# Optimization experiments

Measured on AMD Instinct MI355X. Metric: run time of the kernel, lower is better.

## Reference

```python
import jax, jax.numpy as jnp
import numpy as np

N_QUBITS = 8
EMBED_DIM = 1024
FFN_DIM = 4096


def _apply_1q_batched(state, gate, wire):
    # state: [N] + [2]*n ; gate: [N,2,2] (per-sample)
    n = state.ndim - 1
    N = state.shape[0]
    L = 2 ** wire
    R = 2 ** (n - 1 - wire)
    st = state.reshape(N, L, 2, R)
    st = jnp.einsum('nba,nlar->nlbr', gate, st)
    return st.reshape((N,) + (2,) * n)


def _apply_1q_shared(state, gate, wire):
    # gate: [2,2] shared across samples
    n = state.ndim - 1
    N = state.shape[0]
    L = 2 ** wire
    R = 2 ** (n - 1 - wire)
    st = state.reshape(N, L, 2, R)
    st = jnp.einsum('ba,nlar->nlbr', gate, st)
    return st.reshape((N,) + (2,) * n)


def _cnot(state, control, target):
    c_ax = control + 1
    t_ax = target + 1
    s0 = jnp.take(state, 0, axis=c_ax)
    s1 = jnp.take(state, 1, axis=c_ax)
    t_ax2 = t_ax - 1 if t_ax > c_ax else t_ax  # axis shift after take
    s1 = jnp.flip(s1, axis=t_ax2)
    return jnp.stack([s0, s1], axis=c_ax)


def _simulate(q_inputs, qparams):
    # q_inputs: [N, n_qubits] RX angles; qparams: [n_qubits, 3] Rot(phi,theta,omega)
    N = q_inputs.shape[0]
    n = N_QUBITS
    state = jnp.zeros((N, 2 ** n), dtype=jnp.complex64).at[:, 0].set(1.0)
    state = state.reshape((N,) + (2,) * n)
    # RX layer (per-sample angles)
    half = q_inputs.astype(jnp.float32) * 0.5
    c = jnp.cos(half).astype(jnp.complex64)
    s = (-1j) * jnp.sin(half).astype(jnp.complex64)
    for i in range(n):
        gate = jnp.stack([jnp.stack([c[:, i], s[:, i]], -1),
                          jnp.stack([s[:, i], c[:, i]], -1)], -2)  # [N,2,2]
        state = _apply_1q_batched(state, gate, i)
    # Rot layer: Rot(phi, theta, omega) = RZ(omega) RY(theta) RZ(phi)
    for i in range(n):
        phi, theta, omega = qparams[i, 0], qparams[i, 1], qparams[i, 2]
        ct = jnp.cos(theta / 2).astype(jnp.complex64)
        st = jnp.sin(theta / 2).astype(jnp.complex64)
        ep = jnp.exp(-0.5j * (phi + omega).astype(jnp.complex64))
        em = jnp.exp(0.5j * (phi - omega).astype(jnp.complex64))
        gate = jnp.array(0., jnp.complex64) + jnp.stack([
            jnp.stack([ep * ct, -em * st]),
            jnp.stack([jnp.conj(em) * st, jnp.conj(ep) * ct])])
        state = _apply_1q_shared(state, gate, i)
    # CNOT ring
    for i in range(n - 1):
        state = _cnot(state, i, i + 1)
    state = _cnot(state, n - 1, 0)
    # PauliZ expectations
    probs = jnp.abs(state) ** 2  # [N] + [2]*n, float32
    zs = []
    for i in range(n):
        axes = tuple(a for a in range(1, n + 1) if a != i + 1)
        m = probs.sum(axes)  # [N,2]
        zs.append(m[:, 0] - m[:, 1])
    return jnp.stack(zs, -1)  # [N, n_qubits]


def setup_inputs() -> dict:
    key = jax.random.key(0)
    k = jax.random.split(key, 6)
    x = jax.random.normal(k[0], (4, 2048, EMBED_DIM), dtype=jnp.float32)
    W1 = jax.random.normal(k[1], (FFN_DIM, EMBED_DIM), dtype=jnp.float32) * 0.02
    b1 = jnp.zeros((FFN_DIM,), dtype=jnp.float32)
    qparams = jax.random.normal(k[2], (N_QUBITS, 3), dtype=jnp.float32)
    W2 = jax.random.normal(k[3], (EMBED_DIM, N_QUBITS), dtype=jnp.float32) * 0.02
    b2 = jnp.zeros((EMBED_DIM,), dtype=jnp.float32)
    return {"x": x, "W1": W1, "b1": b1, "qparams": qparams, "W2": W2, "b2": b2}


def reference(x, W1, b1, qparams, W2, b2):
    batch, seq_len, embed_dim = x.shape
    x_flat = x.reshape(-1, embed_dim)
    x_ffn = x_flat @ W1.T + b1                       # [N, ffn_dim]
    q_inputs = x_ffn[:, :N_QUBITS]                   # ffn_dim >= n_qubits
    q_out = _simulate(q_inputs, qparams)             # [N, n_qubits]
    out = q_out @ W2.T + b2                          # [N, embed_dim]
    return out.reshape(batch, seq_len, embed_dim)
```

## Files before the change

### kernel.cpp

```cpp
#include <hip/hip_runtime.h>
#include <math.h>


constexpr int EMBED = 1024;
constexpr int NQ    = 8;
constexpr int BLOCK = 256;
constexpr int WAVES = BLOCK / 64;
constexpr int RPW   = 4;
constexpr float INV2PI = 0.15915494309189535f;

__global__ __launch_bounds__(BLOCK, 2)
void ffq(const float* __restrict__ x,
         const float* __restrict__ W1,
         const float* __restrict__ b1,
         const float* __restrict__ qp,
         const float* __restrict__ W2,
         const float* __restrict__ b2,
         float* __restrict__ out,
         int total_rows)
{
    const int t    = threadIdx.x;
    const int lane = t & 63;
    const int wv   = t >> 6;

    __shared__ float lds_w1[NQ * EMBED];

    {
        const float4* src = reinterpret_cast<const float4*>(W1);
        float4* dst = reinterpret_cast<float4*>(lds_w1);
#pragma unroll
        for (int k = 0; k < (NQ * EMBED / 4) / BLOCK; ++k)
            dst[k * BLOCK + t] = src[k * BLOCK + t];
    }

    const int j = lane & 7;
    float Rj, qoffj;
    {
        const float phi = qp[j * 3 + 0];
        const float th  = qp[j * 3 + 1];
        const float cth  = cosf(th);
        const float ssps = sinf(th) * sinf(phi);
        Rj    = sqrtf(cth * cth + ssps * ssps);
        qoffj = (b1[j] + atan2f(ssps, cth)) * INV2PI;
    }

    float4 w2a[4][4], w2b[4][4];
    float4 b2f[4];
#pragma unroll
    for (int i = 0; i < 4; ++i) {
        const int c = i * 256 + lane * 4;
#pragma unroll
        for (int q = 0; q < 4; ++q) {
            w2a[i][q] = *reinterpret_cast<const float4*>(W2 + (c + q) * NQ);
            w2b[i][q] = *reinterpret_cast<const float4*>(W2 + (c + q) * NQ + 4);
        }
        b2f[i] = *reinterpret_cast<const float4*>(b2 + c);
    }

    __syncthreads();

    const int  gw = blockIdx.x * WAVES + wv;
    const long r0 = (long)gw * RPW;

    float4 xv[4];
    if (r0 < total_rows) {
#pragma unroll
        for (int i = 0; i < 4; ++i)
            xv[i] = *reinterpret_cast<const float4*>(
                x + (size_t)r0 * EMBED + i * 256 + lane * 4);
    }

    for (int rr = 0; rr < RPW; ++rr) {
        const long row = r0 + rr;
        if (row >= total_rows) break;

        float4 xn[4];
        const bool more = (rr + 1 < RPW) && (row + 1 < total_rows);
        if (more) {
#pragma unroll
            for (int i = 0; i < 4; ++i)
                xn[i] = *reinterpret_cast<const float4*>(
                    x + (size_t)(row + 1) * EMBED + i * 256 + lane * 4);
        }

        float p[NQ];
#pragma unroll
        for (int jj = 0; jj < NQ; ++jj) p[jj] = 0.f;
#pragma unroll
        for (int i = 0; i < 4; ++i) {
#pragma unroll
            for (int jj = 0; jj < NQ; ++jj) {
                const float4 w = *reinterpret_cast<const float4*>(
                    lds_w1 + jj * EMBED + i * 256 + lane * 4);
                p[jj] += xv[i].x * w.x + xv[i].y * w.y +
                         xv[i].z * w.z + xv[i].w * w.w;
            }
        }

        float q4[4], q2[2], tsum;
        {
            const bool up = (lane & 4);
#pragma unroll
            for (int k = 0; k < 4; ++k) {
                const float snd = up ? p[k]     : p[k + 4];
                const float kp  = up ? p[k + 4] : p[k];
                q4[k] = kp + __shfl_xor(snd, 4, 64);
            }
        }
        {
            const bool up = (lane & 2);
#pragma unroll
            for (int k = 0; k < 2; ++k) {
                const float snd = up ? q4[k]     : q4[k + 2];
                const float kp  = up ? q4[k + 2] : q4[k];
                q2[k] = kp + __shfl_xor(snd, 2, 64);
            }
        }
        {
            const bool up = (lane & 1);
            const float snd = up ? q2[0] : q2[1];
            const float kp  = up ? q2[1] : q2[0];
            tsum = kp + __shfl_xor(snd, 1, 64);
        }
        tsum += __shfl_xor(tsum, 8, 64);
        tsum += __shfl_xor(tsum, 16, 64);
        tsum += __shfl_xor(tsum, 32, 64);

        const float arg = tsum * INV2PI + qoffj;
        const float zz  = Rj * __builtin_amdgcn_cosf(arg);

        float z0_, z1_, z2_, z3_, z4_, z5_, z6_, z7_;
        {
            const float o  = __shfl_xor(zz, 1, 64);
            const float a0 = (lane & 1) ? o  : zz;
            const float a1 = (lane & 1) ? zz : o;
            const float rA = __shfl_xor(a0, 2, 64);
            const float rB = __shfl_xor(a1, 2, 64);
            const float c0 = (lane & 2) ? rA : a0;
            const float c1 = (lane & 2) ? rB : a1;
            const float c2 = (lane & 2) ? a0 : rA;
            const float c3 = (lane & 2) ? a1 : rB;
            const float d0 = __shfl_xor(c0, 4, 64);
            const float d1 = __shfl_xor(c1, 4, 64);
            const float d2 = __shfl_xor(c2, 4, 64);
            const float d3 = __shfl_xor(c3, 4, 64);
            z0_ = (lane & 4) ? d0 : c0;
            z1_ = (lane & 4) ? d1 : c1;
            z2_ = (lane & 4) ? d2 : c2;
            z3_ = (lane & 4) ? d3 : c3;
            z4_ = (lane & 4) ? c0 : d0;
            z5_ = (lane & 4) ? c1 : d1;
            z6_ = (lane & 4) ? c2 : d2;
            z7_ = (lane & 4) ? c3 : d3;
        }

        float qo0, qo1, qo2, qo3, qo4, qo5, qo6, qo7;
        qo1 = z0_ * z1_;
        qo2 = qo1 * z2_;
        qo3 = qo2 * z3_;
        qo4 = qo3 * z4_;
        qo5 = qo4 * z5_;
        qo6 = qo5 * z6_;
        qo7 = qo6 * z7_;
        qo0 = z1_ * z2_ * z3_ * z4_ * z5_ * z6_ * z7_;

        float* outp = out + (size_t)row * EMBED;
#pragma unroll
        for (int i = 0; i < 4; ++i) {
            float4 o = b2f[i];
            o.x += qo0 * w2a[i][0].x + qo1 * w2a[i][0].y + qo2 * w2a[i][0].z + qo3 * w2a[i][0].w
                 + qo4 * w2b[i][0].x + qo5 * w2b[i][0].y + qo6 * w2b[i][0].z + qo7 * w2b[i][0].w;
            o.y += qo0 * w2a[i][1].x + qo1 * w2a[i][1].y + qo2 * w2a[i][1].z + qo3 * w2a[i][1].w
                 + qo4 * w2b[i][1].x + qo5 * w2b[i][1].y + qo6 * w2b[i][1].z + qo7 * w2b[i][1].w;
            o.z += qo0 * w2a[i][2].x + qo1 * w2a[i][2].y + qo2 * w2a[i][2].z + qo3 * w2a[i][2].w
                 + qo4 * w2b[i][2].x + qo5 * w2b[i][2].y + qo6 * w2b[i][2].z + qo7 * w2b[i][2].w;
            o.w += qo0 * w2a[i][3].x + qo1 * w2a[i][3].y + qo2 * w2a[i][3].z + qo3 * w2a[i][3].w
                 + qo4 * w2b[i][3].x + qo5 * w2b[i][3].y + qo6 * w2b[i][3].z + qo7 * w2b[i][3].w;
            *reinterpret_cast<float4*>(outp + i * 256 + lane * 4) = o;
        }

#pragma unroll
        for (int i = 0; i < 4; ++i) xv[i] = xn[i];
    }
}

extern "C" void kernel_launch(void* const* d_in, const int* in_sizes, int n_in,
                              void* d_out, int out_size, void* d_ws, size_t ws_size,
                              hipStream_t stream) {
    const float* x  = (const float*)d_in[0];
    const float* W1 = (const float*)d_in[1];
    const float* b1 = (const float*)d_in[2];
    const float* qp = (const float*)d_in[3];
    const float* W2 = (const float*)d_in[4];
    const float* b2 = (const float*)d_in[5];
    float* out = (float*)d_out;

    const int rows = in_sizes[0] / EMBED;
    const int rows_per_block = WAVES * RPW;
    const int grid = (rows + rows_per_block - 1) / rows_per_block;

    hipLaunchKernelGGL(ffq, dim3(grid), dim3(BLOCK), 0, stream,
                       x, W1, b1, qp, W2, b2, out, rows);
}
```

Before: 108.1 us.

## Batch four rows per wave and stage transposed W2 in LDS

Each wave now issues all four rows' x loads up front, before the W1 staging, and processes the rows jointly. Every W1 LDS read feeds four rows of FMAs, and W2 is transposed into LDS instead of being held in 32 float4 registers per thread. This aims to get more memory parallelism early and to cut register pressure and LDS traffic per row. The cost is doubled LDS use per block (64KB), which may limit occupancy, plus more live x registers and extra transpose work at block start.

```diff
diff --git a/kernel.cpp b/kernel.cpp
--- a/kernel.cpp
+++ b/kernel.cpp
@@ -5,8 +5,8 @@
 constexpr int EMBED = 1024;
 constexpr int NQ    = 8;
 constexpr int BLOCK = 256;
-constexpr int WAVES = BLOCK / 64;
 constexpr int RPW   = 4;
+constexpr int BR    = 16;
 constexpr float INV2PI = 0.15915494309189535f;
 
 __global__ __launch_bounds__(BLOCK, 2)
@@ -22,88 +22,90 @@
     const int t    = threadIdx.x;
     const int lane = t & 63;
     const int wv   = t >> 6;
-
-    __shared__ float lds_w1[NQ * EMBED];
+    const int j    = lane & 7;
+
+    __shared__ float w1s[NQ * EMBED];
+    __shared__ float w2t[NQ * EMBED];
+
+    const long r0 = (long)blockIdx.x * BR + wv * RPW;
+
+    float4 xv[RPW][4];
+#pragma unroll
+    for (int r = 0; r < RPW; ++r) {
+        long row = r0 + r; if (row >= total_rows) row = total_rows - 1;
+#pragma unroll
+        for (int i = 0; i < 4; ++i)
+            xv[r][i] = *reinterpret_cast<const float4*>(
+                x + (size_t)row * EMBED + i * 256 + lane * 4);
+    }
 
     {
-        const float4* src = reinterpret_cast<const float4*>(W1);
-        float4* dst = reinterpret_cast<float4*>(lds_w1);
+        const float4* w1g = reinterpret_cast<const float4*>(W1);
+        float4* w1d = reinterpret_cast<float4*>(w1s);
 #pragma unroll
         for (int k = 0; k < (NQ * EMBED / 4) / BLOCK; ++k)
-            dst[k * BLOCK + t] = src[k * BLOCK + t];
-    }
-
-    const int j = lane & 7;
+            w1d[k * BLOCK + t] = w1g[k * BLOCK + t];
+#pragma unroll
+        for (int m = 0; m < 4; ++m) {
+            const int col = m * BLOCK + t;
+            const float4 a = *reinterpret_cast<const float4*>(W2 + col * NQ);
+            const float4 b = *reinterpret_cast<const float4*>(W2 + col * NQ + 4);
+            w2t[0 * EMBED + col] = a.x;  w2t[1 * EMBED + col] = a.y;
+            w2t[2 * EMBED + col] = a.z;  w2t[3 * EMBED + col] = a.w;
+            w2t[4 * EMBED + col] = b.x;  w2t[5 * EMBED + col] = b.y;
+            w2t[6 * EMBED + col] = b.z;  w2t[7 * EMBED + col] = b.w;
+        }
+    }
+
     float Rj, qoffj;
     {
-        const float phi = qp[j * 3 + 0];
-        const float th  = qp[j * 3 + 1];
+        const float phi  = qp[j * 3 + 0];
+        const float th   = qp[j * 3 + 1];
         const float cth  = cosf(th);
         const float ssps = sinf(th) * sinf(phi);
         Rj    = sqrtf(cth * cth + ssps * ssps);
         qoffj = (b1[j] + atan2f(ssps, cth)) * INV2PI;
     }
 
-    float4 w2a[4][4], w2b[4][4];
-    float4 b2f[4];
+    float4 b2v[4];
+#pragma unroll
+    for (int i = 0; i < 4; ++i)
+        b2v[i] = *reinterpret_cast<const float4*>(b2 + i * 256 + lane * 4);
+
+    __syncthreads();
+
+    float p[RPW][NQ];
+#pragma unroll
+    for (int r = 0; r < RPW; ++r)
+#pragma unroll
+        for (int jj = 0; jj < NQ; ++jj) p[r][jj] = 0.f;
+
 #pragma unroll
     for (int i = 0; i < 4; ++i) {
-        const int c = i * 256 + lane * 4;
-#pragma unroll
-        for (int q = 0; q < 4; ++q) {
-            w2a[i][q] = *reinterpret_cast<const float4*>(W2 + (c + q) * NQ);
-            w2b[i][q] = *reinterpret_cast<const float4*>(W2 + (c + q) * NQ + 4);
-        }
-        b2f[i] = *reinterpret_cast<const float4*>(b2 + c);
-    }
-
-    __syncthreads();
-
-    const int  gw = blockIdx.x * WAVES + wv;
-    const long r0 = (long)gw * RPW;
-
-    float4 xv[4];
-    if (r0 < total_rows) {
-#pragma unroll
-        for (int i = 0; i < 4; ++i)
-            xv[i] = *reinterpret_cast<const float4*>(
-                x + (size_t)r0 * EMBED + i * 256 + lane * 4);
-    }
-
-    for (int rr = 0; rr < RPW; ++rr) {
-        const long row = r0 + rr;
-        if (row >= total_rows) break;
-
-        float4 xn[4];
-        const bool more = (rr + 1 < RPW) && (row + 1 < total_rows);
-        if (more) {
-#pragma unroll
-            for (int i = 0; i < 4; ++i)
-                xn[i] = *reinterpret_cast<const float4*>(
-                    x + (size_t)(row + 1) * EMBED + i * 256 + lane * 4);
-        }
-
-        float p[NQ];
-#pragma unroll
-        for (int jj = 0; jj < NQ; ++jj) p[jj] = 0.f;
-#pragma unroll
-        for (int i = 0; i < 4; ++i) {
-#pragma unroll
-            for (int jj = 0; jj < NQ; ++jj) {
-                const float4 w = *reinterpret_cast<const float4*>(
-                    lds_w1 + jj * EMBED + i * 256 + lane * 4);
-                p[jj] += xv[i].x * w.x + xv[i].y * w.y +
-                         xv[i].z * w.z + xv[i].w * w.w;
-            }
-        }
-
+#pragma unroll
+        for (int jj = 0; jj < NQ; ++jj) {
+            const float4 w = *reinterpret_cast<const float4*>(
+                w1s + jj * EMBED + i * 256 + lane * 4);
+#pragma unroll
+            for (int r = 0; r < RPW; ++r) {
+                p[r][jj] = fmaf(xv[r][i].x, w.x, p[r][jj]);
+                p[r][jj] = fmaf(xv[r][i].y, w.y, p[r][jj]);
+                p[r][jj] = fmaf(xv[r][i].z, w.z, p[r][jj]);
+                p[r][jj] = fmaf(xv[r][i].w, w.w, p[r][jj]);
+            }
+        }
+    }
+
+    float qo[RPW][NQ];
+#pragma unroll
+    for (int r = 0; r < RPW; ++r) {
         float q4[4], q2[2], tsum;
         {
             const bool up = (lane & 4);
 #pragma unroll
             for (int k = 0; k < 4; ++k) {
-                const float snd = up ? p[k]     : p[k + 4];
-                const float kp  = up ? p[k + 4] : p[k];
+                const float snd = up ? p[r][k]     : p[r][k + 4];
+                const float kp  = up ? p[r][k + 4] : p[r][k];
                 q4[k] = kp + __shfl_xor(snd, 4, 64);
             }
         }
@@ -126,8 +128,7 @@
         tsum += __shfl_xor(tsum, 16, 64);
         tsum += __shfl_xor(tsum, 32, 64);
 
-        const float arg = tsum * INV2PI + qoffj;
-        const float zz  = Rj * __builtin_amdgcn_cosf(arg);
+        const float zz = Rj * __builtin_amdgcn_cosf(tsum * INV2PI + qoffj);
 
         float z0_, z1_, z2_, z3_, z4_, z5_, z6_, z7_;
         {
@@ -154,33 +155,39 @@
             z7_ = (lane & 4) ? c3 : d3;
         }
 
-        float qo0, qo1, qo2, qo3, qo4, qo5, qo6, qo7;
-        qo1 = z0_ * z1_;
-        qo2 = qo1 * z2_;
-        qo3 = qo2 * z3_;
-        qo4 = qo3 * z4_;
-        qo5 = qo4 * z5_;
-        qo6 = qo5 * z6_;
-        qo7 = qo6 * z7_;
-        qo0 = z1_ * z2_ * z3_ * z4_ * z5_ * z6_ * z7_;
-
-        float* outp = out + (size_t)row * EMBED;
-#pragma unroll
-        for (int i = 0; i < 4; ++i) {
-            float4 o = b2f[i];
-            o.x += qo0 * w2a[i][0].x + qo1 * w2a[i][0].y + qo2 * w2a[i][0].z + qo3 * w2a[i][0].w
-                 + qo4 * w2b[i][0].x + qo5 * w2b[i][0].y + qo6 * w2b[i][0].z + qo7 * w2b[i][0].w;
-            o.y += qo0 * w2a[i][1].x + qo1 * w2a[i][1].y + qo2 * w2a[i][1].z + qo3 * w2a[i][1].w
-                 + qo4 * w2b[i][1].x + qo5 * w2b[i][1].y + qo6 * w2b[i][1].z + qo7 * w2b[i][1].w;
-            o.z += qo0 * w2a[i][2].x + qo1 * w2a[i][2].y + qo2 * w2a[i][2].z + qo3 * w2a[i][2].w
-                 + qo4 * w2b[i][2].x + qo5 * w2b[i][2].y + qo6 * w2b[i][2].z + qo7 * w2b[i][2].w;
-            o.w += qo0 * w2a[i][3].x + qo1 * w2a[i][3].y + qo2 * w2a[i][3].z + qo3 * w2a[i][3].w
-                 + qo4 * w2b[i][3].x + qo5 * w2b[i][3].y + qo6 * w2b[i][3].z + qo7 * w2b[i][3].w;
-            *reinterpret_cast<float4*>(outp + i * 256 + lane * 4) = o;
-        }
-
-#pragma unroll
-        for (int i = 0; i < 4; ++i) xv[i] = xn[i];
+        qo[r][1] = z0_ * z1_;
+        qo[r][2] = qo[r][1] * z2_;
+        qo[r][3] = qo[r][2] * z3_;
+        qo[r][4] = qo[r][3] * z4_;
+        qo[r][5] = qo[r][4] * z5_;
+        qo[r][6] = qo[r][5] * z6_;
+        qo[r][7] = qo[r][6] * z7_;
+        qo[r][0] = z1_ * z2_ * z3_ * z4_ * z5_ * z6_ * z7_;
+    }
+
+#pragma unroll
+    for (int i = 0; i < 4; ++i) {
+        float4 w[NQ];
+#pragma unroll
+        for (int jj = 0; jj < NQ; ++jj)
+            w[jj] = *reinterpret_cast<const float4*>(
+                w2t + jj * EMBED + i * 256 + lane * 4);
+
+#pragma unroll
+        for (int r = 0; r < RPW; ++r) {
+            const long row = r0 + r;
+            if (row >= total_rows) continue;
+            float4 o = b2v[i];
+#pragma unroll
+            for (int jj = 0; jj < NQ; ++jj) {
+                o.x = fmaf(qo[r][jj], w[jj].x, o.x);
+                o.y = fmaf(qo[r][jj], w[jj].y, o.y);
+                o.z = fmaf(qo[r][jj], w[jj].z, o.z);
+                o.w = fmaf(qo[r][jj], w[jj].w, o.w);
+            }
+            *reinterpret_cast<float4*>(
+                out + (size_t)row * EMBED + i * 256 + lane * 4) = o;
+        }
     }
 }
 
@@ -196,8 +203,7 @@
     float* out = (float*)d_out;
 
     const int rows = in_sizes[0] / EMBED;
-    const int rows_per_block = WAVES * RPW;
-    const int grid = (rows + rows_per_block - 1) / rows_per_block;
+    const int grid = (rows + BR - 1) / BR;
 
     hipLaunchKernelGGL(ffq, dim3(grid), dim3(BLOCK), 0, stream,
                        x, W1, b1, qp, W2, b2, out, rows);
```

After: 102.0 us. 5.7% less time.
